# Kernel optimization log

Hardware: AMD Instinct MI355X
Metric: run time of the kernel (lower is better)

Reference implementation:

```python
import jax, jax.numpy as jnp
import numpy as np

N_EDGES = 6000
NUM_IMGS = 5  # 1 reference + 4 source views
H = W = 800
NUM_HALF_V = 10  # hardcoded in sample_points_2d


def setup_inputs() -> dict:
    rng = np.random.default_rng(0)
    # 3D edge endpoints in camera space, in front of the camera
    start = rng.normal(0.0, 0.3, (N_EDGES, 3)).astype(np.float32)
    start[:, 2] += 2.5
    d = rng.normal(size=(N_EDGES, 3))
    d /= np.linalg.norm(d, axis=1, keepdims=True)
    length = rng.uniform(0.3, 0.7, (N_EDGES, 1))
    end = (start + d * length).astype(np.float32)
    # num_horizontal = clamp(norm/0.01, 2, 1000) -- integer, no gradient, so
    # the ragged coordinate template is precomputed here (faithful to torch)
    num_h = np.clip((np.linalg.norm(end - start, axis=-1) / 0.01).astype(np.int64), 2, 1000)
    edge_idx_x = np.repeat(np.arange(N_EDGES), num_h)
    begin = np.concatenate(([0], np.cumsum(num_h)[:-1]))
    dx = (np.arange(num_h.sum()) - begin[edge_idx_x]) / (num_h - 1)[edge_idx_x]
    dy = np.arange(NUM_HALF_V) / (NUM_HALF_V - 1)
    dy = np.concatenate((-dy[::-1], dy))  # [20]
    coords_x = np.repeat(dx, 2 * NUM_HALF_V).astype(np.float32)  # [T]
    coords_y = np.tile(dy, int(num_h.sum())).astype(np.float32)  # [T]
    edge_idx = np.repeat(edge_idx_x, 2 * NUM_HALF_V).astype(np.int64)  # [T]
    num_per_edge = (num_h * NUM_HALF_V * 2).astype(np.int64)  # [N]
    imgs = rng.random((NUM_IMGS, H, W)).astype(np.float32)
    intrinsic = np.array([[0.8, 0.0, 0.5], [0.0, 0.8, 0.5], [0.0, 0.0, 1.0]], dtype=np.float32)
    trans = np.zeros((NUM_IMGS - 1, 3, 4), dtype=np.float32)
    for i in range(NUM_IMGS - 1):
        Rt = np.eye(3, 4, dtype=np.float32)
        Rt[:, 3] = rng.normal(0.0, 0.05, 3)
        trans[i] = intrinsic @ Rt
    return {
        'start_points': jnp.asarray(start),
        'end_points': jnp.asarray(end),
        'imgs': jnp.asarray(imgs),
        'transformations': jnp.asarray(trans),
        'intrinsic': jnp.asarray(intrinsic),
        'coords_x': jnp.asarray(coords_x),
        'coords_y': jnp.asarray(coords_y),
        'edge_idx': jnp.asarray(edge_idx),
        'num_per_edge': jnp.asarray(num_per_edge),
    }


def _bilinear(img, uv):
    # img [H,W], uv [T,2] in [0,1); grid_sample(align_corners=False) convention
    Hh, Ww = img.shape
    x = uv[:, 0] * Ww - 0.5
    y = uv[:, 1] * Hh - 0.5
    x0 = jnp.floor(x)
    y0 = jnp.floor(y)
    wx = x - x0
    wy = y - y0
    x0i = jnp.clip(x0.astype(jnp.int32), 0, Ww - 1)
    x1i = jnp.clip(x0i + 1, 0, Ww - 1)
    y0i = jnp.clip(y0.astype(jnp.int32), 0, Hh - 1)
    y1i = jnp.clip(y0i + 1, 0, Hh - 1)
    v00 = img[y0i, x0i]
    v01 = img[y0i, x1i]
    v10 = img[y1i, x0i]
    v11 = img[y1i, x1i]
    return (v00 * (1 - wx) + v01 * wx) * (1 - wy) + (v10 * (1 - wx) + v11 * wx) * wy


def reference(start_points, end_points, imgs, transformations, intrinsic,
              coords_x, coords_y, edge_idx, num_per_edge):
    num_src = imgs.shape[0] - 1
    img_w = imgs.shape[2]
    n_edges = start_points.shape[0]
    # interleave endpoints: [2N,3]
    points_c = jnp.stack([start_points, end_points], axis=1).reshape(-1, 3)

    def sample_template(ep):
        # ep: [N,2,2] projected 2D edge endpoints -> per-coordinate 2D points [T,2]
        p0 = ep[:, 0]
        cur_dir = ep[:, 1] - ep[:, 0]
        dir3 = jnp.concatenate([cur_dir, jnp.zeros_like(cur_dir[:, :1])], axis=1)
        z = jnp.zeros_like(dir3).at[:, 2].set(1.0)
        c = jnp.cross(dir3, z)[:, :2]
        edge_up = c / (jnp.linalg.norm(c, axis=-1, keepdims=True) + 1e-6) * (10.0 / img_w)
        return (cur_dir[edge_idx] * coords_x[:, None]
                + edge_up[edge_idx] * coords_y[:, None]
                + p0[edge_idx])

    # reference view projection (pinhole, normalized coords)
    proj = (intrinsic @ points_c.T).T
    ep1 = (proj[:, :2] / (proj[:, 2:3] + 1e-6)).reshape(-1, 2, 2)
    p2d1 = sample_template(ep1)  # [T,2]
    vm1 = jnp.all((p2d1 > 0) & (p2d1 < 1), axis=-1)
    p2d1 = jnp.clip(p2d1, 0.0, 0.999999)

    # source view projections
    hom = jnp.concatenate([points_c, jnp.ones_like(points_c[:, :1])], axis=1)  # [2N,4]
    projs = jnp.einsum('sij,nj->sni', transformations, hom)
    ep2 = (projs[..., :2] / (projs[..., 2:3] + 1e-6)).reshape(num_src, -1, 2, 2)
    p2d2 = jax.vmap(sample_template)(ep2)  # [S,T,2]
    vm2 = jnp.all((p2d2 > 0) & (p2d2 < 1), axis=-1)
    p2d2 = jnp.clip(p2d2, 0.0, 0.999999)

    # bilinear image sampling (irregular gather)
    s1 = _bilinear(imgs[0], p2d1)  # [T]
    s2 = jax.vmap(_bilinear)(imgs[1:], p2d2)  # [S,T]

    # loss4: per-edge mean squared photometric difference; black-area detection
    cnt = num_per_edge.astype(jnp.float32)
    seg_sum = lambda v: jax.ops.segment_sum(v, edge_idx, num_segments=n_edges)
    diff2 = (s2 - s1[None, :]) ** 2  # [S,T]
    similarity_loss = jax.vmap(seg_sum)(diff2) / cnt[None, :]  # [S,N]
    black_area = (seg_sum((s1 < 0.01).astype(jnp.float32)) / cnt) > 0.5  # [N]

    # scatter_min of per-point validity -> per-edge mask
    sim_mask_pts = (vm1[None, :] & vm2).astype(jnp.int32)  # [S,T]
    seg_min = lambda m: jax.ops.segment_min(m, edge_idx, num_segments=n_edges)
    similarity_mask = jax.vmap(seg_min)(sim_mask_pts).astype(bool)  # [S,N]

    return similarity_loss, similarity_mask, black_area, p2d1, p2d2
```

## Files before the change

kernel.cpp:

```cpp
#include <hip/hip_runtime.h>
#include <math.h>

#define IMG_W   800
#define IMG_PIX (IMG_W * IMG_W)
#define NEDGE   6000
#define NSRC    4
#define NVIEW   5
#define HDR (2 * NSRC * NEDGE + NEDGE)

typedef float vf4 __attribute__((ext_vector_type(4)));
typedef float vf2 __attribute__((ext_vector_type(2)));

struct __attribute__((packed, aligned(4))) f2u { float a, b; };

__device__ __forceinline__ f2u ld2(const float* __restrict__ p) {
    return *(const f2u*)p;
}
__device__ __forceinline__ float rfl(float x) {
    return __uint_as_float((unsigned)__builtin_amdgcn_readfirstlane(
        (int)__float_as_uint(x)));
}
__device__ __forceinline__ void st4(float* p, float a, float b, float c, float d,
                                    bool nt) {
    vf4 v; v.x = a; v.y = b; v.z = c; v.w = d;
    if (nt) __builtin_nontemporal_store(v, (vf4*)p);
    else    *(vf4*)p = v;
}

__global__ void edge_params(const float* __restrict__ sp,
                            const float* __restrict__ epnt,
                            const float* __restrict__ K,
                            const float* __restrict__ T,
                            float4* __restrict__ prm) {
    int e = blockIdx.x * blockDim.x + threadIdx.x;
    if (e >= NEDGE) return;
    float sx = sp[3 * e], sy = sp[3 * e + 1], sz = sp[3 * e + 2];
    float ex = epnt[3 * e], ey = epnt[3 * e + 1], ez = epnt[3 * e + 2];
    for (int v = 0; v < NVIEW; ++v) {
        float as, bs, cs, ae, be, ce;
        if (v == 0) {
            as = K[0] * sx + K[1] * sy + K[2] * sz;
            bs = K[3] * sx + K[4] * sy + K[5] * sz;
            cs = K[6] * sx + K[7] * sy + K[8] * sz;
            ae = K[0] * ex + K[1] * ey + K[2] * ez;
            be = K[3] * ex + K[4] * ey + K[5] * ez;
            ce = K[6] * ex + K[7] * ey + K[8] * ez;
        } else {
            const float* t = T + (v - 1) * 12;
            as = t[0] * sx + t[1] * sy + t[2] * sz + t[3];
            bs = t[4] * sx + t[5] * sy + t[6] * sz + t[7];
            cs = t[8] * sx + t[9] * sy + t[10] * sz + t[11];
            ae = t[0] * ex + t[1] * ey + t[2] * ez + t[3];
            be = t[4] * ex + t[5] * ey + t[6] * ez + t[7];
            ce = t[8] * ex + t[9] * ey + t[10] * ez + t[11];
        }
        float u0 = as / (cs + 1e-6f);
        float w0 = bs / (cs + 1e-6f);
        float u1 = ae / (ce + 1e-6f);
        float w1 = be / (ce + 1e-6f);
        float dx = u1 - u0, dy = w1 - w0;
        float cxx = dy, cyy = -dx;
        float nrm = sqrtf(cxx * cxx + cyy * cyy);
        float inv = 1.f / (nrm + 1e-6f) * (10.0f / (float)IMG_W);
        prm[(e * NVIEW + v) * 2 + 0] = make_float4(u0, w0, dx, dy);
        prm[(e * NVIEW + v) * 2 + 1] = make_float4(cxx * inv, cyy * inv, 0.f, 0.f);
    }
}

__global__ void __launch_bounds__(256)
scan_kernel(const int* __restrict__ npe, int* __restrict__ bg) {
    __shared__ int part[256];
    int t = threadIdx.x;
    int base = t * 24;
    int loc[24];
    int s = 0;
#pragma unroll
    for (int i = 0; i < 24; ++i) {
        int idx = base + i;
        int v = (idx < NEDGE) ? npe[idx] : 0;
        loc[i] = s;
        s += v;
    }
    part[t] = s;
    __syncthreads();
    int own = s;
    for (int off = 1; off < 256; off <<= 1) {
        int v = (t >= off) ? part[t - off] : 0;
        __syncthreads();
        part[t] += v;
        __syncthreads();
    }
    int myoff = part[t] - own;
#pragma unroll
    for (int i = 0; i < 24; ++i) {
        int idx = base + i;
        if (idx < NEDGE) bg[idx] = myoff + loc[i];
    }
}

__global__ void __launch_bounds__(256)
points_kernel(const int* __restrict__ npe,
              const int* __restrict__ bg,
              const float* __restrict__ imgs,
              const float* __restrict__ prm,
              float* __restrict__ out,
              int P) {
    const int e = blockIdx.x;
    const int nsamp = npe[e];
    const int nh = nsamp / 20;
    const int b20 = bg[e];

    __shared__ float DX[1000];
    __shared__ float DY[20];
    __shared__ float rS[4][5];
    __shared__ int   rM[4];

    for (int h = threadIdx.x; h < nh; h += 256)
        DX[h] = (float)((double)h / (double)(nh - 1));
    if (threadIdx.x < 20) {
        int m = threadIdx.x;
        DY[m] = (m < 10) ? -(float)((double)(9 - m) / 9.0)
                         :  (float)((double)(m - 10) / 9.0);
    }

    float Ax[NVIEW], Ay[NVIEW], Az[NVIEW], Aw[NVIEW], Bx[NVIEW], By[NVIEW];
    {
        const float* pe = prm + (size_t)e * (NVIEW * 8);
#pragma unroll
        for (int v = 0; v < NVIEW; ++v) {
            Ax[v] = rfl(pe[8 * v + 0]);
            Ay[v] = rfl(pe[8 * v + 1]);
            Az[v] = rfl(pe[8 * v + 2]);
            Aw[v] = rfl(pe[8 * v + 3]);
            Bx[v] = rfl(pe[8 * v + 4]);
            By[v] = rfl(pe[8 * v + 5]);
        }
    }

    float* vbase[NVIEW];
    bool   val64[NVIEW];
    {
        size_t gb = (size_t)b20;
        vbase[0] = out + HDR + 2 * gb;
#pragma unroll
        for (int s = 0; s < NSRC; ++s)
            vbase[s + 1] = out + HDR + 2 * (size_t)P + 2 * ((size_t)s * P + gb);
#pragma unroll
        for (int v = 0; v < NVIEW; ++v)
            val64[v] = ((((size_t)vbase[v]) & 63) == 0);
    }
    __syncthreads();

    float accs[NSRC] = {0.f, 0.f, 0.f, 0.f};
    float accB = 0.f;
    unsigned maskAcc = 0x1Fu;

    const int t = threadIdx.x;
    for (int base = 0; base < nsamp; base += 512) {
        int p0 = base + 2 * t;
        bool valid = (p0 < nsamp);

        float px[2 * NVIEW], py[2 * NVIEW];
        if (valid) {
#pragma unroll
            for (int k = 0; k < 2; ++k) {
                int p = p0 + k;
                int h = p / 20;
                int m = p - h * 20;
                float xk = DX[h];
                float yk = DY[m];
                unsigned mb = 0;
#pragma unroll
                for (int v = 0; v < NVIEW; ++v) {
                    float ux = Az[v] * xk + Bx[v] * yk + Ax[v];
                    float uy = Aw[v] * xk + By[v] * yk + Ay[v];
                    if ((ux > 0.f) && (ux < 1.f) && (uy > 0.f) && (uy < 1.f))
                        mb |= (1u << v);
                    px[k * NVIEW + v] = fminf(fmaxf(ux, 0.f), 0.999999f);
                    py[k * NVIEW + v] = fminf(fmaxf(uy, 0.f), 0.999999f);
                }
                maskAcc &= mb;
            }

#pragma unroll
            for (int v = 0; v < NVIEW; ++v) {
                st4(vbase[v] + 2 * base + 4 * t,
                    px[0 * NVIEW + v], py[0 * NVIEW + v],
                    px[1 * NVIEW + v], py[1 * NVIEW + v], val64[v]);
            }

            f2u r0[2 * NVIEW], r1[2 * NVIEW];
            unsigned hib = 0;
#pragma unroll
            for (int k = 0; k < 2; ++k) {
#pragma unroll
                for (int v = 0; v < NVIEW; ++v) {
                    int j = k * NVIEW + v;
                    float fx = px[j] * (float)IMG_W - 0.5f;
                    float fy = py[j] * (float)IMG_W - 0.5f;
                    float xf = floorf(fx), yf = floorf(fy);
                    px[j] = fx - xf;
                    py[j] = fy - yf;
                    int x0 = (int)xf;
                    int y0 = (int)yf;
                    int xc = min(max(x0, 0), IMG_W - 2);
                    int y0i = min(max(y0, 0), IMG_W - 1);
                    int y1i = min(y0i + 1, IMG_W - 1);
                    if (x0 >= IMG_W - 1) hib |= (1u << j);
                    const float* im = imgs + v * IMG_PIX;
                    r0[j] = ld2(im + y0i * IMG_W + xc);
                    r1[j] = ld2(im + y1i * IMG_W + xc);
                }
            }
#pragma unroll
            for (int k = 0; k < 2; ++k) {
                float sval[NVIEW];
#pragma unroll
                for (int v = 0; v < NVIEW; ++v) {
                    int j = k * NVIEW + v;
                    bool hi = (hib >> j) & 1u;
                    float v00 = hi ? r0[j].b : r0[j].a;
                    float v01 = r0[j].b;
                    float v10 = hi ? r1[j].b : r1[j].a;
                    float v11 = r1[j].b;
                    float wxv = px[j], wyv = py[j];
                    sval[v] = (v00 * (1.f - wxv) + v01 * wxv) * (1.f - wyv)
                            + (v10 * (1.f - wxv) + v11 * wxv) * wyv;
                }
                float s1 = sval[0];
                accB += (s1 < 0.01f) ? 1.f : 0.f;
#pragma unroll
                for (int s = 0; s < NSRC; ++s) {
                    float d = sval[s + 1] - s1;
                    accs[s] += d * d;
                }
            }
        }
    }

    int lane = threadIdx.x & 63, wid = threadIdx.x >> 6;
    int mi = (int)maskAcc;
#pragma unroll
    for (int off = 32; off > 0; off >>= 1) {
        accs[0] += __shfl_down(accs[0], off);
        accs[1] += __shfl_down(accs[1], off);
        accs[2] += __shfl_down(accs[2], off);
        accs[3] += __shfl_down(accs[3], off);
        accB    += __shfl_down(accB, off);
        mi      &= __shfl_down(mi, off);
    }
    if (lane == 0) {
        rS[wid][0] = accs[0]; rS[wid][1] = accs[1];
        rS[wid][2] = accs[2]; rS[wid][3] = accs[3];
        rS[wid][4] = accB;
        rM[wid] = mi;
    }
    __syncthreads();
    if (threadIdx.x == 0) {
        float s0 = 0.f, s1 = 0.f, s2 = 0.f, s3 = 0.f, sB = 0.f;
        int m = 0x1F;
#pragma unroll
        for (int w = 0; w < 4; ++w) {
            s0 += rS[w][0]; s1 += rS[w][1]; s2 += rS[w][2]; s3 += rS[w][3];
            sB += rS[w][4];
            m  &= rM[w];
        }
        float cnt = (float)nsamp;
        out[0 * NEDGE + e] = s0 / cnt;
        out[1 * NEDGE + e] = s1 / cnt;
        out[2 * NEDGE + e] = s2 / cnt;
        out[3 * NEDGE + e] = s3 / cnt;
        bool vm1 = m & 1;
#pragma unroll
        for (int s = 0; s < NSRC; ++s)
            out[NSRC * NEDGE + s * NEDGE + e] =
                (vm1 && ((m >> (s + 1)) & 1)) ? 1.f : 0.f;
        out[2 * NSRC * NEDGE + e] = ((sB / cnt) > 0.5f) ? 1.f : 0.f;
    }
}

extern "C" void kernel_launch(void* const* d_in, const int* in_sizes, int n_in,
                              void* d_out, int out_size, void* d_ws, size_t ws_size,
                              hipStream_t stream) {
    const float* start = (const float*)d_in[0];
    const float* endp  = (const float*)d_in[1];
    const float* imgs  = (const float*)d_in[2];
    const float* trans = (const float*)d_in[3];
    const float* K     = (const float*)d_in[4];
    const int*   npe   = (const int*)d_in[8];
    int P = in_sizes[5];

    float4* prm = (float4*)d_ws;
    int*    bg  = (int*)((char*)d_ws + NEDGE * NVIEW * 2 * 16);

    float* out = (float*)d_out;
    edge_params<<<(NEDGE + 255) / 256, 256, 0, stream>>>(start, endp, K, trans, prm);
    scan_kernel<<<1, 256, 0, stream>>>(npe, bg);
    points_kernel<<<NEDGE, 256, 0, stream>>>(npe, bg, imgs, (const float*)prm, out, P);
}
```

Measured before the change: 385.0 us.

## Fuse edge-param and scan kernels into points kernel, process four samples per thread

Removes the separate edge_params and scan_kernel launches. Each block now computes its own per-view projection parameters and its output offset through a block-wide reduction over npe[0..e). The main loop also handles four samples per thread per iteration instead of two, so more gathers are in flight at once. In exchange, every block redundantly reads up to 6000 npe values, and register pressure rises.

```diff
diff --git a/kernel.cpp b/kernel.cpp
--- a/kernel.cpp
+++ b/kernel.cpp
@@ -9,16 +9,11 @@
 #define HDR (2 * NSRC * NEDGE + NEDGE)
 
 typedef float vf4 __attribute__((ext_vector_type(4)));
-typedef float vf2 __attribute__((ext_vector_type(2)));
 
 struct __attribute__((packed, aligned(4))) f2u { float a, b; };
 
 __device__ __forceinline__ f2u ld2(const float* __restrict__ p) {
     return *(const f2u*)p;
-}
-__device__ __forceinline__ float rfl(float x) {
-    return __uint_as_float((unsigned)__builtin_amdgcn_readfirstlane(
-        (int)__float_as_uint(x)));
 }
 __device__ __forceinline__ void st4(float* p, float a, float b, float c, float d,
                                     bool nt) {
@@ -27,113 +22,75 @@
     else    *(vf4*)p = v;
 }
 
-__global__ void edge_params(const float* __restrict__ sp,
-                            const float* __restrict__ epnt,
-                            const float* __restrict__ K,
-                            const float* __restrict__ T,
-                            float4* __restrict__ prm) {
-    int e = blockIdx.x * blockDim.x + threadIdx.x;
-    if (e >= NEDGE) return;
-    float sx = sp[3 * e], sy = sp[3 * e + 1], sz = sp[3 * e + 2];
-    float ex = epnt[3 * e], ey = epnt[3 * e + 1], ez = epnt[3 * e + 2];
-    for (int v = 0; v < NVIEW; ++v) {
-        float as, bs, cs, ae, be, ce;
-        if (v == 0) {
-            as = K[0] * sx + K[1] * sy + K[2] * sz;
-            bs = K[3] * sx + K[4] * sy + K[5] * sz;
-            cs = K[6] * sx + K[7] * sy + K[8] * sz;
-            ae = K[0] * ex + K[1] * ey + K[2] * ez;
-            be = K[3] * ex + K[4] * ey + K[5] * ez;
-            ce = K[6] * ex + K[7] * ey + K[8] * ez;
-        } else {
-            const float* t = T + (v - 1) * 12;
-            as = t[0] * sx + t[1] * sy + t[2] * sz + t[3];
-            bs = t[4] * sx + t[5] * sy + t[6] * sz + t[7];
-            cs = t[8] * sx + t[9] * sy + t[10] * sz + t[11];
-            ae = t[0] * ex + t[1] * ey + t[2] * ez + t[3];
-            be = t[4] * ex + t[5] * ey + t[6] * ez + t[7];
-            ce = t[8] * ex + t[9] * ey + t[10] * ez + t[11];
-        }
-        float u0 = as / (cs + 1e-6f);
-        float w0 = bs / (cs + 1e-6f);
-        float u1 = ae / (ce + 1e-6f);
-        float w1 = be / (ce + 1e-6f);
-        float dx = u1 - u0, dy = w1 - w0;
-        float cxx = dy, cyy = -dx;
-        float nrm = sqrtf(cxx * cxx + cyy * cyy);
-        float inv = 1.f / (nrm + 1e-6f) * (10.0f / (float)IMG_W);
-        prm[(e * NVIEW + v) * 2 + 0] = make_float4(u0, w0, dx, dy);
-        prm[(e * NVIEW + v) * 2 + 1] = make_float4(cxx * inv, cyy * inv, 0.f, 0.f);
-    }
-}
-
 __global__ void __launch_bounds__(256)
-scan_kernel(const int* __restrict__ npe, int* __restrict__ bg) {
-    __shared__ int part[256];
-    int t = threadIdx.x;
-    int base = t * 24;
-    int loc[24];
-    int s = 0;
-#pragma unroll
-    for (int i = 0; i < 24; ++i) {
-        int idx = base + i;
-        int v = (idx < NEDGE) ? npe[idx] : 0;
-        loc[i] = s;
-        s += v;
-    }
-    part[t] = s;
-    __syncthreads();
-    int own = s;
-    for (int off = 1; off < 256; off <<= 1) {
-        int v = (t >= off) ? part[t - off] : 0;
-        __syncthreads();
-        part[t] += v;
-        __syncthreads();
-    }
-    int myoff = part[t] - own;
-#pragma unroll
-    for (int i = 0; i < 24; ++i) {
-        int idx = base + i;
-        if (idx < NEDGE) bg[idx] = myoff + loc[i];
-    }
-}
-
-__global__ void __launch_bounds__(256)
-points_kernel(const int* __restrict__ npe,
-              const int* __restrict__ bg,
+points_kernel(const float* __restrict__ sp,
+              const float* __restrict__ epnt,
+              const float* __restrict__ K,
+              const float* __restrict__ T,
+              const int* __restrict__ npe,
               const float* __restrict__ imgs,
-              const float* __restrict__ prm,
               float* __restrict__ out,
               int P) {
     const int e = blockIdx.x;
     const int nsamp = npe[e];
     const int nh = nsamp / 20;
-    const int b20 = bg[e];
+    const int t = threadIdx.x;
+    const int lane = t & 63, wid = t >> 6;
 
     __shared__ float DX[1000];
     __shared__ float DY[20];
     __shared__ float rS[4][5];
     __shared__ int   rM[4];
-
-    for (int h = threadIdx.x; h < nh; h += 256)
+    __shared__ int   redI[4];
+
+    for (int h = t; h < nh; h += 256)
         DX[h] = (float)((double)h / (double)(nh - 1));
-    if (threadIdx.x < 20) {
-        int m = threadIdx.x;
-        DY[m] = (m < 10) ? -(float)((double)(9 - m) / 9.0)
-                         :  (float)((double)(m - 10) / 9.0);
-    }
+    if (t < 20)
+        DY[t] = (t < 10) ? -(float)((double)(9 - t) / 9.0)
+                         :  (float)((double)(t - 10) / 9.0);
+
+    int partial = 0;
+    for (int i = t; i < e; i += 256) partial += npe[i];
+#pragma unroll
+    for (int off = 32; off > 0; off >>= 1)
+        partial += __shfl_down(partial, off);
+    if (lane == 0) redI[wid] = partial;
+    __syncthreads();
+    const int b20 = redI[0] + redI[1] + redI[2] + redI[3];
 
     float Ax[NVIEW], Ay[NVIEW], Az[NVIEW], Aw[NVIEW], Bx[NVIEW], By[NVIEW];
     {
-        const float* pe = prm + (size_t)e * (NVIEW * 8);
+        float sx = sp[3 * e], sy = sp[3 * e + 1], sz = sp[3 * e + 2];
+        float ex = epnt[3 * e], ey = epnt[3 * e + 1], ez = epnt[3 * e + 2];
 #pragma unroll
         for (int v = 0; v < NVIEW; ++v) {
-            Ax[v] = rfl(pe[8 * v + 0]);
-            Ay[v] = rfl(pe[8 * v + 1]);
-            Az[v] = rfl(pe[8 * v + 2]);
-            Aw[v] = rfl(pe[8 * v + 3]);
-            Bx[v] = rfl(pe[8 * v + 4]);
-            By[v] = rfl(pe[8 * v + 5]);
+            float as, bs, cs, ae, be, ce;
+            if (v == 0) {
+                as = K[0] * sx + K[1] * sy + K[2] * sz;
+                bs = K[3] * sx + K[4] * sy + K[5] * sz;
+                cs = K[6] * sx + K[7] * sy + K[8] * sz;
+                ae = K[0] * ex + K[1] * ey + K[2] * ez;
+                be = K[3] * ex + K[4] * ey + K[5] * ez;
+                ce = K[6] * ex + K[7] * ey + K[8] * ez;
+            } else {
+                const float* tt = T + (v - 1) * 12;
+                as = tt[0] * sx + tt[1] * sy + tt[2] * sz + tt[3];
+                bs = tt[4] * sx + tt[5] * sy + tt[6] * sz + tt[7];
+                cs = tt[8] * sx + tt[9] * sy + tt[10] * sz + tt[11];
+                ae = tt[0] * ex + tt[1] * ey + tt[2] * ez + tt[3];
+                be = tt[4] * ex + tt[5] * ey + tt[6] * ez + tt[7];
+                ce = tt[8] * ex + tt[9] * ey + tt[10] * ez + tt[11];
+            }
+            float u0 = as / (cs + 1e-6f);
+            float w0 = bs / (cs + 1e-6f);
+            float u1 = ae / (ce + 1e-6f);
+            float w1 = be / (ce + 1e-6f);
+            float dx = u1 - u0, dy = w1 - w0;
+            float cxx = dy, cyy = -dx;
+            float nrm = sqrtf(cxx * cxx + cyy * cyy);
+            float inv = 1.f / (nrm + 1e-6f) * (10.0f / (float)IMG_W);
+            Ax[v] = u0; Ay[v] = w0; Az[v] = dx; Aw[v] = dy;
+            Bx[v] = cxx * inv; By[v] = cyy * inv;
         }
     }
 
@@ -149,96 +106,103 @@
         for (int v = 0; v < NVIEW; ++v)
             val64[v] = ((((size_t)vbase[v]) & 63) == 0);
     }
-    __syncthreads();
 
     float accs[NSRC] = {0.f, 0.f, 0.f, 0.f};
     float accB = 0.f;
     unsigned maskAcc = 0x1Fu;
 
-    const int t = threadIdx.x;
-    for (int base = 0; base < nsamp; base += 512) {
-        int p0 = base + 2 * t;
-        bool valid = (p0 < nsamp);
-
-        float px[2 * NVIEW], py[2 * NVIEW];
-        if (valid) {
-#pragma unroll
-            for (int k = 0; k < 2; ++k) {
-                int p = p0 + k;
-                int h = p / 20;
-                int m = p - h * 20;
-                float xk = DX[h];
-                float yk = DY[m];
-                unsigned mb = 0;
-#pragma unroll
-                for (int v = 0; v < NVIEW; ++v) {
-                    float ux = Az[v] * xk + Bx[v] * yk + Ax[v];
-                    float uy = Aw[v] * xk + By[v] * yk + Ay[v];
-                    if ((ux > 0.f) && (ux < 1.f) && (uy > 0.f) && (uy < 1.f))
-                        mb |= (1u << v);
-                    px[k * NVIEW + v] = fminf(fmaxf(ux, 0.f), 0.999999f);
-                    py[k * NVIEW + v] = fminf(fmaxf(uy, 0.f), 0.999999f);
-                }
-                maskAcc &= mb;
-            }
-
+    for (int base = 0; base < nsamp; base += 1024) {
+        int q0 = base + 2 * t;
+        int q1 = base + 512 + 2 * t;
+        bool v0 = (q0 < nsamp);
+        bool v1 = (q1 < nsamp);
+
+        float px[4 * NVIEW], py[4 * NVIEW];
+#pragma unroll
+        for (int k = 0; k < 4; ++k) {
+            bool ok = (k < 2) ? v0 : v1;
+            if (!ok) continue;
+            int p = ((k < 2) ? q0 : q1) + (k & 1);
+            int h = p / 20;
+            int m = p - h * 20;
+            float xk = DX[h];
+            float yk = DY[m];
+            unsigned mb = 0;
 #pragma unroll
             for (int v = 0; v < NVIEW; ++v) {
-                st4(vbase[v] + 2 * base + 4 * t,
-                    px[0 * NVIEW + v], py[0 * NVIEW + v],
-                    px[1 * NVIEW + v], py[1 * NVIEW + v], val64[v]);
-            }
-
-            f2u r0[2 * NVIEW], r1[2 * NVIEW];
-            unsigned hib = 0;
-#pragma unroll
-            for (int k = 0; k < 2; ++k) {
-#pragma unroll
-                for (int v = 0; v < NVIEW; ++v) {
-                    int j = k * NVIEW + v;
-                    float fx = px[j] * (float)IMG_W - 0.5f;
-                    float fy = py[j] * (float)IMG_W - 0.5f;
-                    float xf = floorf(fx), yf = floorf(fy);
-                    px[j] = fx - xf;
-                    py[j] = fy - yf;
-                    int x0 = (int)xf;
-                    int y0 = (int)yf;
-                    int xc = min(max(x0, 0), IMG_W - 2);
-                    int y0i = min(max(y0, 0), IMG_W - 1);
-                    int y1i = min(y0i + 1, IMG_W - 1);
-                    if (x0 >= IMG_W - 1) hib |= (1u << j);
-                    const float* im = imgs + v * IMG_PIX;
-                    r0[j] = ld2(im + y0i * IMG_W + xc);
-                    r1[j] = ld2(im + y1i * IMG_W + xc);
-                }
-            }
-#pragma unroll
-            for (int k = 0; k < 2; ++k) {
-                float sval[NVIEW];
-#pragma unroll
-                for (int v = 0; v < NVIEW; ++v) {
-                    int j = k * NVIEW + v;
-                    bool hi = (hib >> j) & 1u;
-                    float v00 = hi ? r0[j].b : r0[j].a;
-                    float v01 = r0[j].b;
-                    float v10 = hi ? r1[j].b : r1[j].a;
-                    float v11 = r1[j].b;
-                    float wxv = px[j], wyv = py[j];
-                    sval[v] = (v00 * (1.f - wxv) + v01 * wxv) * (1.f - wyv)
-                            + (v10 * (1.f - wxv) + v11 * wxv) * wyv;
-                }
-                float s1 = sval[0];
-                accB += (s1 < 0.01f) ? 1.f : 0.f;
-#pragma unroll
-                for (int s = 0; s < NSRC; ++s) {
-                    float d = sval[s + 1] - s1;
-                    accs[s] += d * d;
-                }
-            }
-        }
-    }
-
-    int lane = threadIdx.x & 63, wid = threadIdx.x >> 6;
+                float ux = Az[v] * xk + Bx[v] * yk + Ax[v];
+                float uy = Aw[v] * xk + By[v] * yk + Ay[v];
+                if ((ux > 0.f) && (ux < 1.f) && (uy > 0.f) && (uy < 1.f))
+                    mb |= (1u << v);
+                px[k * NVIEW + v] = fminf(fmaxf(ux, 0.f), 0.999999f);
+                py[k * NVIEW + v] = fminf(fmaxf(uy, 0.f), 0.999999f);
+            }
+            maskAcc &= mb;
+        }
+
+#pragma unroll
+        for (int v = 0; v < NVIEW; ++v) {
+            float* bp = vbase[v] + 2 * base;
+            if (v0) st4(bp + 4 * t,
+                        px[0 * NVIEW + v], py[0 * NVIEW + v],
+                        px[1 * NVIEW + v], py[1 * NVIEW + v], val64[v]);
+            if (v1) st4(bp + 1024 + 4 * t,
+                        px[2 * NVIEW + v], py[2 * NVIEW + v],
+                        px[3 * NVIEW + v], py[3 * NVIEW + v], val64[v]);
+        }
+
+        f2u r0[4 * NVIEW], r1[4 * NVIEW];
+        unsigned hib = 0;
+#pragma unroll
+        for (int k = 0; k < 4; ++k) {
+            bool ok = (k < 2) ? v0 : v1;
+            if (!ok) continue;
+#pragma unroll
+            for (int v = 0; v < NVIEW; ++v) {
+                int j = k * NVIEW + v;
+                float fx = px[j] * (float)IMG_W - 0.5f;
+                float fy = py[j] * (float)IMG_W - 0.5f;
+                float xf = floorf(fx), yf = floorf(fy);
+                px[j] = fx - xf;
+                py[j] = fy - yf;
+                int x0 = (int)xf;
+                int y0 = (int)yf;
+                int xc = min(max(x0, 0), IMG_W - 2);
+                int y0i = min(max(y0, 0), IMG_W - 1);
+                int y1i = min(y0i + 1, IMG_W - 1);
+                if (x0 >= IMG_W - 1) hib |= (1u << j);
+                const float* im = imgs + v * IMG_PIX;
+                r0[j] = ld2(im + y0i * IMG_W + xc);
+                r1[j] = ld2(im + y1i * IMG_W + xc);
+            }
+        }
+#pragma unroll
+        for (int k = 0; k < 4; ++k) {
+            bool ok = (k < 2) ? v0 : v1;
+            if (!ok) continue;
+            float sval[NVIEW];
+#pragma unroll
+            for (int v = 0; v < NVIEW; ++v) {
+                int j = k * NVIEW + v;
+                bool hi = (hib >> j) & 1u;
+                float v00 = hi ? r0[j].b : r0[j].a;
+                float v01 = r0[j].b;
+                float v10 = hi ? r1[j].b : r1[j].a;
+                float v11 = r1[j].b;
+                float wxv = px[j], wyv = py[j];
+                sval[v] = (v00 * (1.f - wxv) + v01 * wxv) * (1.f - wyv)
+                        + (v10 * (1.f - wxv) + v11 * wxv) * wyv;
+            }
+            float s1 = sval[0];
+            accB += (s1 < 0.01f) ? 1.f : 0.f;
+#pragma unroll
+            for (int s = 0; s < NSRC; ++s) {
+                float d = sval[s + 1] - s1;
+                accs[s] += d * d;
+            }
+        }
+    }
+
     int mi = (int)maskAcc;
 #pragma unroll
     for (int off = 32; off > 0; off >>= 1) {
@@ -256,7 +220,7 @@
         rM[wid] = mi;
     }
     __syncthreads();
-    if (threadIdx.x == 0) {
+    if (t == 0) {
         float s0 = 0.f, s1 = 0.f, s2 = 0.f, s3 = 0.f, sB = 0.f;
         int m = 0x1F;
 #pragma unroll
@@ -290,11 +254,7 @@
     const int*   npe   = (const int*)d_in[8];
     int P = in_sizes[5];
 
-    float4* prm = (float4*)d_ws;
-    int*    bg  = (int*)((char*)d_ws + NEDGE * NVIEW * 2 * 16);
-
     float* out = (float*)d_out;
-    edge_params<<<(NEDGE + 255) / 256, 256, 0, stream>>>(start, endp, K, trans, prm);
-    scan_kernel<<<1, 256, 0, stream>>>(npe, bg);
-    points_kernel<<<NEDGE, 256, 0, stream>>>(npe, bg, imgs, (const float*)prm, out, P);
-}
+    points_kernel<<<NEDGE, 256, 0, stream>>>(start, endp, K, trans, npe, imgs,
+                                             out, P);
+}
```

After: 415.1 us. +7.8%, slower.
